# Optimization experiments

Hardware: AMD Instinct MI355X
Metric: run time of the kernel (lower is better)

Reference implementation:

```python
import jax, jax.numpy as jnp
import numpy as np

GRID = 32
SCALE_FACTOR = 0.2
EPS = 1e-12


def _compute_phi(verts, faces, G):
    """Unsigned distance-to-mesh on a GxGxG grid over [-1,1]^3, zeroed outside the mesh.
    Returns phi[z, y, x] (grid_sample D,H,W layout). verts [V,3], faces [F,3] int.
    Matches the SDF CUDA kernel semantics: phi = penetration depth (dist inside, 0 outside)."""
    v0 = verts[faces[:, 0]]  # [F,3]
    v1 = verts[faces[:, 1]]
    v2 = verts[faces[:, 2]]
    e0 = v1 - v0             # [F,3]
    e1 = v2 - v0
    a = jnp.sum(e0 * e0, -1)             # [F]
    b = jnp.sum(e0 * e1, -1)
    c = jnp.sum(e1 * e1, -1)

    lin = jnp.linspace(-1.0, 1.0, G, dtype=verts.dtype)
    zz, yy, xx = jnp.meshgrid(lin, lin, lin, indexing='ij')
    pts = jnp.stack([xx, yy, zz], -1).reshape(-1, 3)   # [P,3], coords (x,y,z), P=G^3

    # --- point-to-triangle squared distance, all [P,F] after one [P,F,3] temp ---
    w = pts[:, None, :] - v0[None, :, :]               # [P,F,3]
    f = jnp.sum(w * w, -1)                             # |p-v0|^2   [P,F]
    de0 = jnp.sum(w * e0, -1)                          # (p-v0).e0  [P,F]
    de1 = jnp.sum(w * e1, -1)                          # (p-v0).e1  [P,F]

    det = a * c - b * b                                # [F]
    det_s = jnp.where(det > EPS, det, 1.0)
    u = (c * de0 - b * de1) / det_s                    # barycentric of plane projection
    v = (a * de1 - b * de0) / det_s
    inside_tri = (u >= 0) & (v >= 0) & (u + v <= 1) & (det > EPS)
    plane_d2 = f - (u * de0 + v * de1)                 # squared dist to plane point

    # edge v0->v1
    a_s = jnp.where(a > EPS, a, 1.0)
    t0 = jnp.clip(de0 / a_s, 0.0, 1.0)
    d2_0 = f - 2.0 * t0 * de0 + t0 * t0 * a
    # edge v0->v2
    c_s = jnp.where(c > EPS, c, 1.0)
    t1 = jnp.clip(de1 / c_s, 0.0, 1.0)
    d2_1 = f - 2.0 * t1 * de1 + t1 * t1 * c
    # edge v1->v2: e2 = e1-e0; w1 = p - v1 = w - e0
    ee2 = a + c - 2.0 * b                              # |e2|^2
    ee2_s = jnp.where(ee2 > EPS, ee2, 1.0)
    dot2 = de1 - de0 - (b - a)                         # w1.e2
    w1sq = f - 2.0 * de0 + a                           # |w1|^2
    t2 = jnp.clip(dot2 / ee2_s, 0.0, 1.0)
    d2_2 = w1sq - 2.0 * t2 * dot2 + t2 * t2 * ee2

    edge_d2 = jnp.minimum(jnp.minimum(d2_0, d2_1), d2_2)
    d2 = jnp.where(inside_tri, plane_d2, edge_d2)
    d2 = jnp.maximum(d2, 0.0)
    dist = jnp.sqrt(jnp.min(d2, axis=1))               # [P]

    # --- inside/outside via +z ray casting parity ---
    x0, y0, z0 = v0[:, 0], v0[:, 1], v0[:, 2]
    x1, y1, z1 = v1[:, 0], v1[:, 1], v1[:, 2]
    x2, y2, z2 = v2[:, 0], v2[:, 1], v2[:, 2]
    det2 = (x1 - x0) * (y2 - y0) - (x2 - x0) * (y1 - y0)   # [F]
    det2_s = jnp.where(jnp.abs(det2) > EPS, det2, 1.0)
    px = pts[:, 0:1]; py = pts[:, 1:2]; pz = pts[:, 2:3]   # [P,1]
    u2 = ((px - x0) * (y2 - y0) - (py - y0) * (x2 - x0)) / det2_s  # [P,F]
    v2b = ((x1 - x0) * (py - y0) - (y1 - y0) * (px - x0)) / det2_s
    in2d = (u2 >= 0) & (v2b >= 0) & (u2 + v2b <= 1) & (jnp.abs(det2) > EPS)
    zint = z0 + u2 * (z1 - z0) + v2b * (z2 - z0)
    hits = jnp.sum((in2d & (zint > pz)).astype(jnp.int32), axis=1)  # [P]
    inside_mesh = (hits % 2).astype(dist.dtype)

    phi = dist * inside_mesh                           # >= 0 everywhere
    return phi.reshape(G, G, G)                        # [z, y, x]


def _trilinear_zeros(phi, q):
    """torch grid_sample(mode=bilinear, padding=zeros, align_corners=True) on a
    [G,G,G] (z,y,x) volume at points q [N,3] with coords (x,y,z) in [-1,1]."""
    G = phi.shape[0]
    fidx = (q + 1.0) * 0.5 * (G - 1)                   # [N,3] float indices (x,y,z)
    i0 = jnp.floor(fidx).astype(jnp.int32)
    w1 = fidx - i0.astype(fidx.dtype)
    w0 = 1.0 - w1
    out = jnp.zeros(q.shape[0], dtype=phi.dtype)
    for dz in (0, 1):
        for dy in (0, 1):
            for dx in (0, 1):
                ix = i0[:, 0] + dx
                iy = i0[:, 1] + dy
                iz = i0[:, 2] + dz
                valid = (ix >= 0) & (ix < G) & (iy >= 0) & (iy < G) & (iz >= 0) & (iz < G)
                val = phi[jnp.clip(iz, 0, G - 1), jnp.clip(iy, 0, G - 1), jnp.clip(ix, 0, G - 1)]
                wgt = ((w1[:, 0] if dx else w0[:, 0]) *
                       (w1[:, 1] if dy else w0[:, 1]) *
                       (w1[:, 2] if dz else w0[:, 2]))
                out = out + jnp.where(valid, val * wgt, 0.0)
    return out


def _sdf_loss(human_verts, object_verts, faces):
    sg = jax.lax.stop_gradient
    # bounding boxes (computed under no_grad in the original)
    bmin_h = jnp.min(human_verts, axis=0); bmax_h = jnp.max(human_verts, axis=0)
    bmin_o = jnp.min(object_verts, axis=0); bmax_o = jnp.max(object_verts, axis=0)
    overlap = jnp.all(bmin_h <= bmax_o) & jnp.all(bmin_o <= bmax_h)

    center = sg(0.5 * (bmin_h + bmax_h))                               # [3]
    scale = sg((1.0 + SCALE_FACTOR) * 0.5 * jnp.max(bmax_h - bmin_h))  # scalar

    hv_scaled = sg((human_verts - center) / scale)      # in [-1,1]^3 by construction
    phi = sg(_compute_phi(hv_scaled, faces, GRID))      # [G,G,G], no_grad in original

    q = (object_verts - center) / scale                 # grads flow to object_verts
    phi_val = _trilinear_zeros(phi, q)                  # [N]
    loss = jnp.sum(phi_val) ** 2
    return jnp.where(overlap, loss, jnp.zeros((), dtype=loss.dtype))


def setup_inputs() -> dict:
    key = jax.random.key(0)
    k1, k2, k3 = jax.random.split(key, 3)
    human_verts = jax.random.normal(k1, (778, 3), dtype=jnp.float32)
    object_verts = jax.random.normal(k2, (4096, 3), dtype=jnp.float32)
    faces = jax.random.randint(k3, (1538, 3), 0, 778, dtype=jnp.int32)
    return {"human_verts": human_verts, "object_verts": object_verts, "faces": faces}


def reference(human_verts, object_verts, faces):
    return _sdf_loss(human_verts, object_verts, faces)
```

## Files before the change

### kernel.cpp

```cpp
#include <hip/hip_runtime.h>

#define EPSF 1e-12f
#define GN 32
#define NPTS (GN * GN * GN)
#define NCOL (GN * GN)
#define FSPLIT 16
#define NCG 16
#define NBLK (NCG * FSPLIT)
#define NTHR 1024
#define MAXCH 160
#define CAP 8192
#define POISON 0xAAAAAAAAu

__device__ __forceinline__ float dot_rn(const float* x, const float* y) {
    return __fadd_rn(__fadd_rn(__fmul_rn(x[0], y[0]), __fmul_rn(x[1], y[1])),
                     __fmul_rn(x[2], y[2]));
}
__device__ __forceinline__ float wmin64(float v) {
    for (int o = 32; o > 0; o >>= 1) v = fminf(v, __shfl_xor(v, o));
    return v;
}
__device__ __forceinline__ float wmax64(float v) {
    for (int o = 32; o > 0; o >>= 1) v = fmaxf(v, __shfl_xor(v, o));
    return v;
}
__device__ __forceinline__ float wsum64(float v) {
    for (int o = 32; o > 0; o >>= 1) v += __shfl_xor(v, o);
    return v;
}
__device__ __forceinline__ float gridc(int g) {
    return __fadd_rn(-1.0f, __fmul_rn((float)g, 2.0f / 31.0f));
}

__device__ __forceinline__ void frec(const float* __restrict__ hv,
                                     const int* __restrict__ faces, int f,
                                     float cx, float cy, float cz, float sc,
                                     float* o) {
    const float qnan = __int_as_float(0x7FC00000);
    int ia = faces[3 * f + 0], ib = faces[3 * f + 1], ic = faces[3 * f + 2];
    float v0[3], v1[3], v2[3];
    for (int k = 0; k < 3; ++k) {
        float cen = (k == 0) ? cx : ((k == 1) ? cy : cz);
        v0[k] = __fdiv_rn(__fsub_rn(hv[3 * ia + k], cen), sc);
        v1[k] = __fdiv_rn(__fsub_rn(hv[3 * ib + k], cen), sc);
        v2[k] = __fdiv_rn(__fsub_rn(hv[3 * ic + k], cen), sc);
    }
    float e0[3], e1[3];
    for (int k = 0; k < 3; ++k) {
        e0[k] = __fsub_rn(v1[k], v0[k]);
        e1[k] = __fsub_rn(v2[k], v0[k]);
    }
    float a = dot_rn(e0, e0);
    float b = dot_rn(e0, e1);
    float cc = dot_rn(e1, e1);
    float det = __fsub_rn(__fmul_rn(a, cc), __fmul_rn(b, b));
    float inv_det = (det > EPSF) ? (1.0f / det) : qnan;
    float inv_a = 1.0f / ((a > EPSF) ? a : 1.0f);
    float inv_c = 1.0f / ((cc > EPSF) ? cc : 1.0f);
    float ee2 = __fsub_rn(__fadd_rn(a, cc), __fmul_rn(2.0f, b));
    float inv_ee2 = 1.0f / ((ee2 > EPSF) ? ee2 : 1.0f);
    float det2 = __fsub_rn(__fmul_rn(e0[0], e1[1]), __fmul_rn(e1[0], e0[1]));
    float inv_det2s = (fabsf(det2) > EPSF) ? (1.0f / det2) : qnan;
    o[0] = v0[0]; o[1] = v0[1]; o[2] = v0[2];
    o[3] = e0[0]; o[4] = e0[1]; o[5] = e0[2];
    o[6] = e1[0]; o[7] = e1[1]; o[8] = e1[2];
    o[9] = a; o[10] = b; o[11] = cc;
    o[12] = inv_det; o[13] = inv_a; o[14] = inv_c;
    o[15] = ee2; o[16] = inv_ee2; o[17] = inv_det2s;
    o[18] = __fsub_rn(b, a); o[19] = 0.f;
}

__device__ __forceinline__ float celld2(const float* r, float px, float py, float pz) {
    float wx = __fsub_rn(px, r[0]), wy = __fsub_rn(py, r[1]), wz = __fsub_rn(pz, r[2]);
    float ff = wx * wx + wy * wy + wz * wz;
    float de0 = wx * r[3] + wy * r[4] + wz * r[5];
    float de1 = wx * r[6] + wy * r[7] + wz * r[8];
    float u = (r[11] * de0 - r[10] * de1) * r[12];
    float v = (r[9] * de1 - r[10] * de0) * r[12];
    bool inside = (u >= 0.0f) & (v >= 0.0f) & (u + v <= 1.0f);
    float plane_d2 = ff - (u * de0 + v * de1);
    float t0 = fminf(fmaxf(de0 * r[13], 0.0f), 1.0f);
    float d2_0 = ff + t0 * (t0 * r[9] - 2.0f * de0);
    float t1 = fminf(fmaxf(de1 * r[14], 0.0f), 1.0f);
    float d2_1 = ff + t1 * (t1 * r[11] - 2.0f * de1);
    float dot2 = (de1 - de0) - r[18];
    float w1sq = ff - 2.0f * de0 + r[9];
    float t2 = fminf(fmaxf(dot2 * r[16], 0.0f), 1.0f);
    float d2_2 = w1sq + t2 * (t2 * r[15] - 2.0f * dot2);
    float ed2 = fminf(fminf(d2_0, d2_1), d2_2);
    float d2 = inside ? plane_d2 : ed2;
    return fmaxf(d2, 0.0f);
}

__global__ void __launch_bounds__(NTHR) k_all(
    const float* __restrict__ hv, int nh,
    const float* __restrict__ ov, int no,
    const int* __restrict__ faces, int nf,
    unsigned* __restrict__ d2u, unsigned* __restrict__ parm,
    unsigned* __restrict__ counter, float* __restrict__ out)
{
    __shared__ float s_fd[MAXCH * 20];
    __shared__ unsigned s_sm[NCOL];
    __shared__ unsigned s_clist[CAP];
    __shared__ unsigned s_cnt[16];
    __shared__ unsigned s_pm[64];
    __shared__ unsigned s_dm[64];
    __shared__ float s_w[16][12];
    __shared__ float s_hdr[4];
    __shared__ float s_hb[6];
    __shared__ unsigned s_last;

    int t = threadIdx.x, lane = t & 63, wvid = t >> 6;
    int fs = blockIdx.x >> 4;
    int cg = blockIdx.x & 15;
    const float step = 2.0f / 31.0f;

    for (int i = t; i < NCOL; i += NTHR) s_sm[i] = 0u;
    if (t < 64) s_pm[t] = 0u;

    {
        float mnx = INFINITY, mny = INFINITY, mnz = INFINITY;
        float mxx = -INFINITY, mxy = -INFINITY, mxz = -INFINITY;
        for (int i = t; i < nh; i += NTHR) {
            float x = hv[3 * i], y = hv[3 * i + 1], z = hv[3 * i + 2];
            mnx = fminf(mnx, x); mny = fminf(mny, y); mnz = fminf(mnz, z);
            mxx = fmaxf(mxx, x); mxy = fmaxf(mxy, y); mxz = fmaxf(mxz, z);
        }
        mnx = wmin64(mnx); mny = wmin64(mny); mnz = wmin64(mnz);
        mxx = wmax64(mxx); mxy = wmax64(mxy); mxz = wmax64(mxz);
        if (lane == 0) {
            s_w[wvid][0] = mnx; s_w[wvid][1] = mny; s_w[wvid][2] = mnz;
            s_w[wvid][3] = mxx; s_w[wvid][4] = mxy; s_w[wvid][5] = mxz;
        }
        __syncthreads();
        if (wvid == 0) {
            float a0 = (lane < 16) ? s_w[lane][0] : INFINITY;
            float a1 = (lane < 16) ? s_w[lane][1] : INFINITY;
            float a2 = (lane < 16) ? s_w[lane][2] : INFINITY;
            float a3 = (lane < 16) ? s_w[lane][3] : -INFINITY;
            float a4 = (lane < 16) ? s_w[lane][4] : -INFINITY;
            float a5 = (lane < 16) ? s_w[lane][5] : -INFINITY;
            a0 = wmin64(a0); a1 = wmin64(a1); a2 = wmin64(a2);
            a3 = wmax64(a3); a4 = wmax64(a4); a5 = wmax64(a5);
            if (lane == 0) {
                float e0 = __fsub_rn(a3, a0);
                float e1 = __fsub_rn(a4, a1);
                float e2 = __fsub_rn(a5, a2);
                float m = fmaxf(e0, fmaxf(e1, e2));
                s_hdr[0] = __fmul_rn(0.5f, __fadd_rn(a0, a3));
                s_hdr[1] = __fmul_rn(0.5f, __fadd_rn(a1, a4));
                s_hdr[2] = __fmul_rn(0.5f, __fadd_rn(a2, a5));
                s_hdr[3] = __fmul_rn(0.6f, m);
                s_hb[0] = a0; s_hb[1] = a1; s_hb[2] = a2;
                s_hb[3] = a3; s_hb[4] = a4; s_hb[5] = a5;
            }
        }
        __syncthreads();
    }
    float cx = s_hdr[0], cy = s_hdr[1], cz = s_hdr[2], sc = s_hdr[3];

    int chunkB = (nf + FSPLIT - 1) / FSPLIT;
    int f0B = fs * chunkB;
    int nloc = min(nf, f0B + chunkB) - f0B;
    for (int i = t; i < nloc; i += NTHR)
        frec(hv, faces, f0B + i, cx, cy, cz, sc, s_fd + i * 20);
    for (int j = t; j < no; j += NTHR) {
        float qx = __fdiv_rn(__fsub_rn(ov[3 * j + 0], cx), sc);
        float qy = __fdiv_rn(__fsub_rn(ov[3 * j + 1], cy), sc);
        float qz = __fdiv_rn(__fsub_rn(ov[3 * j + 2], cz), sc);
        float fx = __fmul_rn(__fmul_rn(__fadd_rn(qx, 1.0f), 0.5f), 31.0f);
        float fy = __fmul_rn(__fmul_rn(__fadd_rn(qy, 1.0f), 0.5f), 31.0f);
        float fz = __fmul_rn(__fmul_rn(__fadd_rn(qz, 1.0f), 0.5f), 31.0f);
        int ix0 = (int)floorf(fx), iy0 = (int)floorf(fy), iz0 = (int)floorf(fz);
        unsigned zb = 0u;
        if ((iz0 >= 0) & (iz0 < GN)) zb |= 1u << iz0;
        if ((iz0 + 1 >= 0) & (iz0 + 1 < GN)) zb |= 1u << (iz0 + 1);
        if (zb) {
            for (int dy = 0; dy < 2; ++dy)
                for (int dx = 0; dx < 2; ++dx) {
                    int ix = ix0 + dx, iy = iy0 + dy;
                    if ((ix >= 0) & (ix < GN) & (iy >= 0) & (iy < GN))
                        atomicOr(&s_sm[iy * GN + ix], zb);
                }
        }
    }
    __syncthreads();

    {
        int col = cg * 64 + lane;
        int gx = col & 31, gy = col >> 5;
        float px = __fadd_rn(-1.0f, __fmul_rn((float)gx, step));
        float py = __fadd_rn(-1.0f, __fmul_rn((float)gy, step));
        int i0 = __builtin_amdgcn_readfirstlane((wvid * nloc) / 16);
        int i1 = __builtin_amdgcn_readfirstlane(((wvid + 1) * nloc) / 16);

        unsigned cmask = 0u;
        for (int i = i0; i < i1; ++i) {
            const float* q = s_fd + i * 20;
            float v0x = q[0], v0y = q[1], v0z = q[2];
            float e0x = q[3], e0y = q[4], e0z = q[5];
            float e1x = q[6], e1y = q[7], e1z = q[8];
            float inv_det2s = q[17];

            float wx = __fsub_rn(px, v0x), wy = __fsub_rn(py, v0y);
            float u2n = __fsub_rn(__fmul_rn(wx, e1y), __fmul_rn(wy, e1x));
            float v2n = __fsub_rn(__fmul_rn(e0x, wy), __fmul_rn(e0y, wx));
            float u2 = __fmul_rn(u2n, inv_det2s);
            float v2 = __fmul_rn(v2n, inv_det2s);
            bool in2d = (u2 >= 0.0f) & (v2 >= 0.0f) & (__fadd_rn(u2, v2) <= 1.0f);
            float zint = __fadd_rn(__fadd_rn(v0z, __fmul_rn(u2, e0z)), __fmul_rn(v2, e1z));
            int c = 0;
            {
                float p;
                p = __fadd_rn(-1.0f, __fmul_rn((float)(15), step));      if (zint > p) c = 16;
                p = __fadd_rn(-1.0f, __fmul_rn((float)(c + 7), step));   if (zint > p) c += 8;
                p = __fadd_rn(-1.0f, __fmul_rn((float)(c + 3), step));   if (zint > p) c += 4;
                p = __fadd_rn(-1.0f, __fmul_rn((float)(c + 1), step));   if (zint > p) c += 2;
                p = __fadd_rn(-1.0f, __fmul_rn((float)(c), step));       if (zint > p) c += 1;
                p = __fadd_rn(-1.0f, __fmul_rn((float)(c), step));       if (zint > p) c += 1;
            }
            unsigned mask = (c == 0) ? 0u : (0xffffffffu >> (32 - c));
            cmask ^= in2d ? mask : 0u;
        }
        atomicXor(&s_pm[lane], cmask);
        __syncthreads();
        if (t < 64) atomicXor(&parm[cg * 64 + t], s_pm[t]);
    }

    unsigned nc;
    {
        unsigned cnt = 0;
        for (int chunk = wvid * 32; chunk < wvid * 32 + 32; ++chunk) {
            unsigned cid = (unsigned)(chunk * 64 + lane);
            bool present = (s_sm[cid >> 5] >> (cid & 31u)) & 1u;
            cnt += (unsigned)__popcll(__ballot(present));
        }
        if (lane == 0) s_cnt[wvid] = cnt;
        __syncthreads();
        unsigned base = 0;
        for (int wv = 0; wv < wvid; ++wv) base += s_cnt[wv];
        nc = base;
        for (int wv = wvid; wv < 16; ++wv) nc += s_cnt[wv];
        if (nc <= CAP) {
            for (int chunk = wvid * 32; chunk < wvid * 32 + 32; ++chunk) {
                unsigned cid = (unsigned)(chunk * 64 + lane);
                bool present = (s_sm[cid >> 5] >> (cid & 31u)) & 1u;
                unsigned long long bal = __ballot(present);
                unsigned pre = (unsigned)__popcll(bal & ((1ull << lane) - 1ull));
                if (present) s_clist[base + pre] = cid;
                base += (unsigned)__popcll(bal);
            }
        }
        __syncthreads();
    }

    {
        bool uselist = nc <= CAP;
        unsigned nbatch = uselist ? ((nc + 63) >> 6) : (NPTS / 64);
        int i0 = __builtin_amdgcn_readfirstlane((wvid * nloc) / 16);
        int i1 = __builtin_amdgcn_readfirstlane(((wvid + 1) * nloc) / 16);

        for (unsigned cb = (unsigned)cg; cb < nbatch; cb += 16) {
            if (t < 64) s_dm[t] = 0x7f800000u;
            __syncthreads();
            unsigned idx = cb * 64 + (unsigned)lane;
            bool cvalid; unsigned cid;
            if (uselist) { cvalid = idx < nc; cid = cvalid ? s_clist[idx] : 0u; }
            else { cid = idx; cvalid = (s_sm[cid >> 5] >> (cid & 31u)) & 1u; }
            int gx = (int)((cid >> 5) & 31u), gy = (int)(cid >> 10),
                gz = (int)(cid & 31u);
            float px = gridc(gx), py = gridc(gy), pz = gridc(gz);
            float dmin = 3.402823466e38f;
            for (int i = i0; i < i1; ++i)
                dmin = fminf(dmin, celld2(s_fd + i * 20, px, py, pz));
            if (cvalid) atomicMin(&s_dm[lane], __float_as_uint(dmin));
            __syncthreads();
            if (t < 64) {
                unsigned idx2 = cb * 64 + (unsigned)t;
                bool v2; unsigned c2;
                if (uselist) { v2 = idx2 < nc; c2 = v2 ? s_clist[idx2] : 0u; }
                else { c2 = idx2; v2 = (s_sm[c2 >> 5] >> (c2 & 31u)) & 1u; }
                if (v2) atomicMin(&d2u[c2], s_dm[t]);
            }
            __syncthreads();
        }
    }

    __syncthreads();
    if (t == 0) {
        unsigned old = atomicAdd(counter, 1u);
        s_last = (old == POISON + (unsigned)(NBLK - 1) - 1u + 1u - 1u ||
                  old == POISON + (unsigned)(NBLK - 1)) ? 0u : 0u;
        s_last = (old == POISON + (unsigned)(NBLK - 1)) ? 1u : 0u;
    }
    __syncthreads();
    if (s_last == 0u) return;

    {
        float onx = INFINITY, ony = INFINITY, onz = INFINITY;
        float oxx = -INFINITY, oxy = -INFINITY, oxz = -INFINITY;
        for (int j = t; j < no; j += NTHR) {
            float x = ov[3 * j], y = ov[3 * j + 1], z = ov[3 * j + 2];
            onx = fminf(onx, x); ony = fminf(ony, y); onz = fminf(onz, z);
            oxx = fmaxf(oxx, x); oxy = fmaxf(oxy, y); oxz = fmaxf(oxz, z);
        }
        onx = wmin64(onx); ony = wmin64(ony); onz = wmin64(onz);
        oxx = wmax64(oxx); oxy = wmax64(oxy); oxz = wmax64(oxz);
        if (lane == 0) {
            s_w[wvid][0] = onx; s_w[wvid][1] = ony; s_w[wvid][2] = onz;
            s_w[wvid][3] = oxx; s_w[wvid][4] = oxy; s_w[wvid][5] = oxz;
        }
        __syncthreads();
        if (t == 0) {
            float a0 = INFINITY, a1 = INFINITY, a2 = INFINITY;
            float a3 = -INFINITY, a4 = -INFINITY, a5 = -INFINITY;
            for (int wv = 0; wv < 16; ++wv) {
                a0 = fminf(a0, s_w[wv][0]); a1 = fminf(a1, s_w[wv][1]);
                a2 = fminf(a2, s_w[wv][2]); a3 = fmaxf(a3, s_w[wv][3]);
                a4 = fmaxf(a4, s_w[wv][4]); a5 = fmaxf(a5, s_w[wv][5]);
            }
            bool ovl = (s_hb[0] <= a3) && (s_hb[1] <= a4) && (s_hb[2] <= a5) &&
                       (a0 <= s_hb[3]) && (a1 <= s_hb[4]) && (a2 <= s_hb[5]);
            s_hdr[0] = ovl ? 1.0f : 0.0f;
        }
        __syncthreads();
        float ovl = s_hdr[0];
        float acc = 0.0f;
        for (int j = t; j < no; j += NTHR) {
            float qx = __fdiv_rn(__fsub_rn(ov[3 * j + 0], cx), sc);
            float qy = __fdiv_rn(__fsub_rn(ov[3 * j + 1], cy), sc);
            float qz = __fdiv_rn(__fsub_rn(ov[3 * j + 2], cz), sc);
            float fx = __fmul_rn(__fmul_rn(__fadd_rn(qx, 1.0f), 0.5f), 31.0f);
            float fy = __fmul_rn(__fmul_rn(__fadd_rn(qy, 1.0f), 0.5f), 31.0f);
            float fz = __fmul_rn(__fmul_rn(__fadd_rn(qz, 1.0f), 0.5f), 31.0f);
            float flx = floorf(fx), fly = floorf(fy), flz = floorf(fz);
            int ix0 = (int)flx, iy0 = (int)fly, iz0 = (int)flz;
            float w1x = __fsub_rn(fx, flx), w0x = __fsub_rn(1.0f, w1x);
            float w1y = __fsub_rn(fy, fly), w0y = __fsub_rn(1.0f, w1y);
            float w1z = __fsub_rn(fz, flz), w0z = __fsub_rn(1.0f, w1z);
            for (int dy = 0; dy < 2; ++dy)
                for (int dx = 0; dx < 2; ++dx) {
                    int ix = ix0 + dx, iy = iy0 + dy;
                    bool okxy = (ix >= 0) & (ix < GN) & (iy >= 0) & (iy < GN);
                    unsigned pm = 0u;
                    if (okxy) {
                        unsigned pmv = __hip_atomic_load(&parm[iy * GN + ix],
                                         __ATOMIC_RELAXED, __HIP_MEMORY_SCOPE_AGENT);
                        pm = pmv ^ POISON;
                    }
                    for (int dz = 0; dz < 2; ++dz) {
                        int iz = iz0 + dz;
                        bool ok = okxy & (iz >= 0) & (iz < GN);
                        if (ok && ((pm >> iz) & 1u)) {
                            unsigned cid = (unsigned)((iy * GN + ix) * GN + iz);
                            unsigned du = __hip_atomic_load(&d2u[cid],
                                __ATOMIC_RELAXED, __HIP_MEMORY_SCOPE_AGENT);
                            float val = sqrtf(__uint_as_float(du));
                            float wgt = __fmul_rn(
                                __fmul_rn(dx ? w1x : w0x, dy ? w1y : w0y),
                                dz ? w1z : w0z);
                            acc = __fadd_rn(acc, __fmul_rn(val, wgt));
                        }
                    }
                }
        }
        acc = wsum64(acc);
        if (lane == 0) s_w[wvid][6] = acc;
        __syncthreads();
        if (wvid == 0) {
            float v = (lane < 16) ? s_w[lane][6] : 0.0f;
            v = wsum64(v);
            if (lane == 0) {
                float loss = __fmul_rn(v, v);
                out[0] = (ovl != 0.0f) ? loss : 0.0f;
            }
        }
    }
}

extern "C" void kernel_launch(void* const* d_in, const int* in_sizes, int n_in,
                              void* d_out, int out_size, void* d_ws, size_t ws_size,
                              hipStream_t stream) {
    const float* hv = (const float*)d_in[0];
    const float* ov = (const float*)d_in[1];
    const int* faces = (const int*)d_in[2];
    int nh = in_sizes[0] / 3;
    int no = in_sizes[1] / 3;
    int nf = in_sizes[2] / 3;

    unsigned* d2u = (unsigned*)d_ws;
    unsigned* parm = d2u + NPTS;
    unsigned* counter = parm + NCOL;

    k_all<<<NBLK, NTHR, 0, stream>>>(hv, nh, ov, no, faces, nf,
                                     d2u, parm, counter, (float*)d_out);
}
```

Measured before the change: 106.3 us.

## Split candidate cells across waves, drop per-batch barriers, hoist tail loads

The distance phase now gives each wave its own candidate-cell batches and loops over all local faces, writing straight to global with atomicMin. This removes the per-batch shared-memory min reduction and its two block barriers. The object bounding-box overlap test moves into the first object-voxelisation pass instead of a second pass in the last block. The tail block stages the cell mask in LDS and issues all eight trilinear corner loads unconditionally with clamped indices, so they can be in flight together. In exchange each wave covers whole batches, which can leave work unbalanced when there are few candidate cells, and global atomics rise by up to a factor of the wave count.

Result: slower. 112.5 us (+5.8%).

```diff
diff --git a/kernel.cpp b/kernel.cpp
--- a/kernel.cpp
+++ b/kernel.cpp
@@ -30,6 +30,9 @@
 }
 __device__ __forceinline__ float gridc(int g) {
     return __fadd_rn(-1.0f, __fmul_rn((float)g, 2.0f / 31.0f));
+}
+__device__ __forceinline__ int clampi(int v, int lo, int hi) {
+    return v < lo ? lo : (v > hi ? hi : v);
 }
 
 __device__ __forceinline__ void frec(const float* __restrict__ hv,
@@ -104,10 +107,10 @@
     __shared__ unsigned s_clist[CAP];
     __shared__ unsigned s_cnt[16];
     __shared__ unsigned s_pm[64];
-    __shared__ unsigned s_dm[64];
     __shared__ float s_w[16][12];
     __shared__ float s_hdr[4];
     __shared__ float s_hb[6];
+    __shared__ float s_ovl;
     __shared__ unsigned s_last;
 
     int t = threadIdx.x, lane = t & 63, wvid = t >> 6;
@@ -164,27 +167,52 @@
     int nloc = min(nf, f0B + chunkB) - f0B;
     for (int i = t; i < nloc; i += NTHR)
         frec(hv, faces, f0B + i, cx, cy, cz, sc, s_fd + i * 20);
-    for (int j = t; j < no; j += NTHR) {
-        float qx = __fdiv_rn(__fsub_rn(ov[3 * j + 0], cx), sc);
-        float qy = __fdiv_rn(__fsub_rn(ov[3 * j + 1], cy), sc);
-        float qz = __fdiv_rn(__fsub_rn(ov[3 * j + 2], cz), sc);
-        float fx = __fmul_rn(__fmul_rn(__fadd_rn(qx, 1.0f), 0.5f), 31.0f);
-        float fy = __fmul_rn(__fmul_rn(__fadd_rn(qy, 1.0f), 0.5f), 31.0f);
-        float fz = __fmul_rn(__fmul_rn(__fadd_rn(qz, 1.0f), 0.5f), 31.0f);
-        int ix0 = (int)floorf(fx), iy0 = (int)floorf(fy), iz0 = (int)floorf(fz);
-        unsigned zb = 0u;
-        if ((iz0 >= 0) & (iz0 < GN)) zb |= 1u << iz0;
-        if ((iz0 + 1 >= 0) & (iz0 + 1 < GN)) zb |= 1u << (iz0 + 1);
-        if (zb) {
-            for (int dy = 0; dy < 2; ++dy)
-                for (int dx = 0; dx < 2; ++dx) {
-                    int ix = ix0 + dx, iy = iy0 + dy;
-                    if ((ix >= 0) & (ix < GN) & (iy >= 0) & (iy < GN))
-                        atomicOr(&s_sm[iy * GN + ix], zb);
-                }
+    {
+        float onx = INFINITY, ony = INFINITY, onz = INFINITY;
+        float oxx = -INFINITY, oxy = -INFINITY, oxz = -INFINITY;
+        for (int j = t; j < no; j += NTHR) {
+            float x = ov[3 * j + 0], y = ov[3 * j + 1], z = ov[3 * j + 2];
+            onx = fminf(onx, x); ony = fminf(ony, y); onz = fminf(onz, z);
+            oxx = fmaxf(oxx, x); oxy = fmaxf(oxy, y); oxz = fmaxf(oxz, z);
+            float qx = __fdiv_rn(__fsub_rn(x, cx), sc);
+            float qy = __fdiv_rn(__fsub_rn(y, cy), sc);
+            float qz = __fdiv_rn(__fsub_rn(z, cz), sc);
+            float fx = __fmul_rn(__fmul_rn(__fadd_rn(qx, 1.0f), 0.5f), 31.0f);
+            float fy = __fmul_rn(__fmul_rn(__fadd_rn(qy, 1.0f), 0.5f), 31.0f);
+            float fz = __fmul_rn(__fmul_rn(__fadd_rn(qz, 1.0f), 0.5f), 31.0f);
+            int ix0 = (int)floorf(fx), iy0 = (int)floorf(fy), iz0 = (int)floorf(fz);
+            unsigned zb = 0u;
+            if ((iz0 >= 0) & (iz0 < GN)) zb |= 1u << iz0;
+            if ((iz0 + 1 >= 0) & (iz0 + 1 < GN)) zb |= 1u << (iz0 + 1);
+            if (zb) {
+                for (int dy = 0; dy < 2; ++dy)
+                    for (int dx = 0; dx < 2; ++dx) {
+                        int ix = ix0 + dx, iy = iy0 + dy;
+                        if ((ix >= 0) & (ix < GN) & (iy >= 0) & (iy < GN))
+                            atomicOr(&s_sm[iy * GN + ix], zb);
+                    }
+            }
+        }
+        onx = wmin64(onx); ony = wmin64(ony); onz = wmin64(onz);
+        oxx = wmax64(oxx); oxy = wmax64(oxy); oxz = wmax64(oxz);
+        if (lane == 0) {
+            s_w[wvid][6] = onx; s_w[wvid][7] = ony; s_w[wvid][8] = onz;
+            s_w[wvid][9] = oxx; s_w[wvid][10] = oxy; s_w[wvid][11] = oxz;
         }
     }
     __syncthreads();
+    if (t == 0) {
+        float a0 = INFINITY, a1 = INFINITY, a2 = INFINITY;
+        float a3 = -INFINITY, a4 = -INFINITY, a5 = -INFINITY;
+        for (int wv = 0; wv < 16; ++wv) {
+            a0 = fminf(a0, s_w[wv][6]); a1 = fminf(a1, s_w[wv][7]);
+            a2 = fminf(a2, s_w[wv][8]); a3 = fmaxf(a3, s_w[wv][9]);
+            a4 = fmaxf(a4, s_w[wv][10]); a5 = fmaxf(a5, s_w[wv][11]);
+        }
+        bool ovl = (s_hb[0] <= a3) && (s_hb[1] <= a4) && (s_hb[2] <= a5) &&
+                   (a0 <= s_hb[3]) && (a1 <= s_hb[4]) && (a2 <= s_hb[5]);
+        s_ovl = ovl ? 1.0f : 0.0f;
+    }
 
     {
         int col = cg * 64 + lane;
@@ -257,12 +285,8 @@
     {
         bool uselist = nc <= CAP;
         unsigned nbatch = uselist ? ((nc + 63) >> 6) : (NPTS / 64);
-        int i0 = __builtin_amdgcn_readfirstlane((wvid * nloc) / 16);
-        int i1 = __builtin_amdgcn_readfirstlane(((wvid + 1) * nloc) / 16);
-
-        for (unsigned cb = (unsigned)cg; cb < nbatch; cb += 16) {
-            if (t < 64) s_dm[t] = 0x7f800000u;
-            __syncthreads();
+        for (unsigned cb = (unsigned)cg + 16u * (unsigned)wvid; cb < nbatch;
+             cb += 256u) {
             unsigned idx = cb * 64 + (unsigned)lane;
             bool cvalid; unsigned cid;
             if (uselist) { cvalid = idx < nc; cid = cvalid ? s_clist[idx] : 0u; }
@@ -271,60 +295,25 @@
                 gz = (int)(cid & 31u);
             float px = gridc(gx), py = gridc(gy), pz = gridc(gz);
             float dmin = 3.402823466e38f;
-            for (int i = i0; i < i1; ++i)
+            for (int i = 0; i < nloc; ++i)
                 dmin = fminf(dmin, celld2(s_fd + i * 20, px, py, pz));
-            if (cvalid) atomicMin(&s_dm[lane], __float_as_uint(dmin));
-            __syncthreads();
-            if (t < 64) {
-                unsigned idx2 = cb * 64 + (unsigned)t;
-                bool v2; unsigned c2;
-                if (uselist) { v2 = idx2 < nc; c2 = v2 ? s_clist[idx2] : 0u; }
-                else { c2 = idx2; v2 = (s_sm[c2 >> 5] >> (c2 & 31u)) & 1u; }
-                if (v2) atomicMin(&d2u[c2], s_dm[t]);
-            }
-            __syncthreads();
+            if (cvalid) atomicMin(&d2u[cid], __float_as_uint(dmin));
         }
     }
 
     __syncthreads();
     if (t == 0) {
         unsigned old = atomicAdd(counter, 1u);
-        s_last = (old == POISON + (unsigned)(NBLK - 1) - 1u + 1u - 1u ||
-                  old == POISON + (unsigned)(NBLK - 1)) ? 0u : 0u;
         s_last = (old == POISON + (unsigned)(NBLK - 1)) ? 1u : 0u;
     }
     __syncthreads();
     if (s_last == 0u) return;
 
     {
-        float onx = INFINITY, ony = INFINITY, onz = INFINITY;
-        float oxx = -INFINITY, oxy = -INFINITY, oxz = -INFINITY;
-        for (int j = t; j < no; j += NTHR) {
-            float x = ov[3 * j], y = ov[3 * j + 1], z = ov[3 * j + 2];
-            onx = fminf(onx, x); ony = fminf(ony, y); onz = fminf(onz, z);
-            oxx = fmaxf(oxx, x); oxy = fmaxf(oxy, y); oxz = fmaxf(oxz, z);
-        }
-        onx = wmin64(onx); ony = wmin64(ony); onz = wmin64(onz);
-        oxx = wmax64(oxx); oxy = wmax64(oxy); oxz = wmax64(oxz);
-        if (lane == 0) {
-            s_w[wvid][0] = onx; s_w[wvid][1] = ony; s_w[wvid][2] = onz;
-            s_w[wvid][3] = oxx; s_w[wvid][4] = oxy; s_w[wvid][5] = oxz;
-        }
-        __syncthreads();
-        if (t == 0) {
-            float a0 = INFINITY, a1 = INFINITY, a2 = INFINITY;
-            float a3 = -INFINITY, a4 = -INFINITY, a5 = -INFINITY;
-            for (int wv = 0; wv < 16; ++wv) {
-                a0 = fminf(a0, s_w[wv][0]); a1 = fminf(a1, s_w[wv][1]);
-                a2 = fminf(a2, s_w[wv][2]); a3 = fmaxf(a3, s_w[wv][3]);
-                a4 = fmaxf(a4, s_w[wv][4]); a5 = fmaxf(a5, s_w[wv][5]);
-            }
-            bool ovl = (s_hb[0] <= a3) && (s_hb[1] <= a4) && (s_hb[2] <= a5) &&
-                       (a0 <= s_hb[3]) && (a1 <= s_hb[4]) && (a2 <= s_hb[5]);
-            s_hdr[0] = ovl ? 1.0f : 0.0f;
-        }
-        __syncthreads();
-        float ovl = s_hdr[0];
+        float ovl = s_ovl;
+        s_sm[t] = __hip_atomic_load(&parm[t], __ATOMIC_RELAXED,
+                                    __HIP_MEMORY_SCOPE_AGENT) ^ POISON;
+        __syncthreads();
         float acc = 0.0f;
         for (int j = t; j < no; j += NTHR) {
             float qx = __fdiv_rn(__fsub_rn(ov[3 * j + 0], cx), sc);
@@ -338,24 +327,28 @@
             float w1x = __fsub_rn(fx, flx), w0x = __fsub_rn(1.0f, w1x);
             float w1y = __fsub_rn(fy, fly), w0y = __fsub_rn(1.0f, w1y);
             float w1z = __fsub_rn(fz, flz), w0z = __fsub_rn(1.0f, w1z);
+            int xc0 = clampi(ix0, 0, 31), xc1 = clampi(ix0 + 1, 0, 31);
+            int yc0 = clampi(iy0, 0, 31), yc1 = clampi(iy0 + 1, 0, 31);
+            int zc0 = clampi(iz0, 0, 31), zc1 = clampi(iz0 + 1, 0, 31);
+            unsigned du[8];
+#pragma unroll
+            for (int k = 0; k < 8; ++k) {
+                int xx = (k & 1) ? xc1 : xc0;
+                int yy = ((k >> 1) & 1) ? yc1 : yc0;
+                int zz = (k >> 2) ? zc1 : zc0;
+                du[k] = __hip_atomic_load(&d2u[(yy * GN + xx) * GN + zz],
+                            __ATOMIC_RELAXED, __HIP_MEMORY_SCOPE_AGENT);
+            }
             for (int dy = 0; dy < 2; ++dy)
                 for (int dx = 0; dx < 2; ++dx) {
                     int ix = ix0 + dx, iy = iy0 + dy;
                     bool okxy = (ix >= 0) & (ix < GN) & (iy >= 0) & (iy < GN);
-                    unsigned pm = 0u;
-                    if (okxy) {
-                        unsigned pmv = __hip_atomic_load(&parm[iy * GN + ix],
-                                         __ATOMIC_RELAXED, __HIP_MEMORY_SCOPE_AGENT);
-                        pm = pmv ^ POISON;
-                    }
+                    unsigned pm = okxy ? s_sm[iy * GN + ix] : 0u;
                     for (int dz = 0; dz < 2; ++dz) {
                         int iz = iz0 + dz;
                         bool ok = okxy & (iz >= 0) & (iz < GN);
                         if (ok && ((pm >> iz) & 1u)) {
-                            unsigned cid = (unsigned)((iy * GN + ix) * GN + iz);
-                            unsigned du = __hip_atomic_load(&d2u[cid],
-                                __ATOMIC_RELAXED, __HIP_MEMORY_SCOPE_AGENT);
-                            float val = sqrtf(__uint_as_float(du));
+                            float val = sqrtf(__uint_as_float(du[dz * 4 + dy * 2 + dx]));
                             float wgt = __fmul_rn(
                                 __fmul_rn(dx ? w1x : w0x, dy ? w1y : w0y),
                                 dz ? w1z : w0z);
@@ -365,10 +358,10 @@
                 }
         }
         acc = wsum64(acc);
-        if (lane == 0) s_w[wvid][6] = acc;
+        if (lane == 0) s_w[wvid][0] = acc;
         __syncthreads();
         if (wvid == 0) {
-            float v = (lane < 16) ? s_w[lane][6] : 0.0f;
+            float v = (lane < 16) ? s_w[lane][0] : 0.0f;
             v = wsum64(v);
             if (lane == 0) {
                 float loss = __fmul_rn(v, v);
```
